# Kernel tuning notes

Measured on AMD Instinct MI355X. Metric: run time of the kernel, lower is better.

## Reference

```python
import jax, jax.numpy as jnp
import numpy as np

N_NODES = 50000
BN_EPS = 1e-5


def setup_inputs() -> dict:
    key = jax.random.key(0)
    ks = jax.random.split(key, 6)
    N, E, CIN, CH, COUT = N_NODES, 800000, 128, 256, 128
    node_feat = jax.random.normal(ks[0], (N, CIN), dtype=jnp.float32)
    edge_index = jax.random.randint(ks[1], (2, E), 0, N, dtype=jnp.int64)
    # Glorot-ish init for weights
    W1 = jax.random.normal(ks[2], (CIN, CH), dtype=jnp.float32) / np.sqrt(CIN)
    b1 = jnp.zeros((CH,), dtype=jnp.float32)
    bn_gamma = jnp.ones((CH,), dtype=jnp.float32)
    bn_beta = jnp.zeros((CH,), dtype=jnp.float32)
    W2 = jax.random.normal(ks[3], (CH, COUT), dtype=jnp.float32) / np.sqrt(CH)
    b2 = jnp.zeros((COUT,), dtype=jnp.float32)
    return {"node_feat": node_feat, "edge_index": edge_index, "W1": W1, "b1": b1,
            "bn_gamma": bn_gamma, "bn_beta": bn_beta, "W2": W2, "b2": b2}


def gcn_conv(x, W, b, src, dst, n_nodes):
    """PyG GCNConv: out = D^-1/2 (A+I) D^-1/2 (x W) + b."""
    h = x @ W                                   # [N, C_out]
    loop = jnp.arange(n_nodes, dtype=src.dtype)
    src_f = jnp.concatenate([src, loop])        # self-loops appended
    dst_f = jnp.concatenate([dst, loop])
    deg = jax.ops.segment_sum(jnp.ones_like(dst_f, dtype=h.dtype), dst_f,
                              num_segments=n_nodes)
    dinv = jax.lax.rsqrt(jnp.maximum(deg, 1.0))  # deg >= 1 due to self-loops
    norm = dinv[src_f] * dinv[dst_f]             # [E+N]
    msg = h[src_f] * norm[:, None]               # gather + scale
    return jax.ops.segment_sum(msg, dst_f, num_segments=n_nodes) + b


def batch_norm(x, gamma, beta):
    mean = jnp.mean(x, axis=0)
    var = jnp.mean((x - mean) ** 2, axis=0)      # biased var (torch BN normalization)
    return (x - mean) * jax.lax.rsqrt(var + BN_EPS) * gamma + beta


def reference(node_feat, edge_index, W1, b1, bn_gamma, bn_beta, W2, b2):
    src, dst = edge_index[0], edge_index[1]
    x = gcn_conv(node_feat, W1, b1, src, dst, N_NODES)
    x = batch_norm(x, bn_gamma, bn_beta)
    x = jax.nn.relu(x)
    # dropout is identity at inference
    x = gcn_conv(x, W2, b2, src, dst, N_NODES)
    return x
```

## Files before the change

### kernel.cpp

```cpp
#include <hip/hip_runtime.h>

#define CIN 128
#define CH 256
#define COUT 128
#define BN_EPS 1e-5f

typedef __attribute__((ext_vector_type(8))) short bf16x8;
typedef __attribute__((ext_vector_type(4))) float f32x4;

__device__ __forceinline__ short f2bf(float x) {
    unsigned u = __float_as_uint(x);
    unsigned r = (u + 0x7fffu + ((u >> 16) & 1u)) >> 16;
    return (short)r;
}
__device__ __forceinline__ float bf2f(short h) {
    return __uint_as_float(((unsigned)(unsigned short)h) << 16);
}

__device__ __forceinline__ void gather_edges(const short* __restrict__ xb,
                                             const uint2* __restrict__ csr,
                                             int e0, int e1, int c,
                                             float* acc) {
    int e = e0;
    for (; e + 7 < e1; e += 8) {
        uint2 ew[8];
        #pragma unroll
        for (int i = 0; i < 8; ++i) ew[i] = csr[e + i];
        bf16x8 x[8];
        #pragma unroll
        for (int i = 0; i < 8; ++i) x[i] = *(const bf16x8*)(xb + (size_t)ew[i].y * 128 + c * 8);
        #pragma unroll
        for (int i = 0; i < 8; ++i) {
            float w = __uint_as_float(ew[i].x);
            #pragma unroll
            for (int j = 0; j < 8; ++j) acc[j] = fmaf(w, bf2f(x[i][j]), acc[j]);
        }
    }
    for (; e + 3 < e1; e += 4) {
        uint2 ew[4];
        #pragma unroll
        for (int i = 0; i < 4; ++i) ew[i] = csr[e + i];
        bf16x8 x[4];
        #pragma unroll
        for (int i = 0; i < 4; ++i) x[i] = *(const bf16x8*)(xb + (size_t)ew[i].y * 128 + c * 8);
        #pragma unroll
        for (int i = 0; i < 4; ++i) {
            float w = __uint_as_float(ew[i].x);
            #pragma unroll
            for (int j = 0; j < 8; ++j) acc[j] = fmaf(w, bf2f(x[i][j]), acc[j]);
        }
    }
    for (; e < e1; ++e) {
        uint2 ew = csr[e];
        float w = __uint_as_float(ew.x);
        bf16x8 x0 = *(const bf16x8*)(xb + (size_t)ew.y * 128 + c * 8);
        #pragma unroll
        for (int j = 0; j < 8; ++j) acc[j] = fmaf(w, bf2f(x0[j]), acc[j]);
    }
}

__global__ void k_deg(const int* __restrict__ dst, int* __restrict__ degi,
                      unsigned short* __restrict__ rank, int E) {
    int e = blockIdx.x * 256 + threadIdx.x;
    if (e < E) rank[e] = (unsigned short)atomicAdd(&degi[dst[e]], 1);
}

__global__ void k_scan1(const int* __restrict__ degi, float* __restrict__ dinv,
                        int* __restrict__ blocksum, int* __restrict__ hist, int N) {
    __shared__ int s[256];
    __shared__ int h[256];
    int tid = threadIdx.x;
    h[tid] = 0;
    int i = blockIdx.x * 256 + tid;
    int v = (i < N) ? degi[i] : 0;
    if (i < N) dinv[i] = rsqrtf((float)(v + 1));
    s[tid] = v;
    __syncthreads();
    if (i < N) atomicAdd(&h[v > 255 ? 255 : v], 1);
    for (int st = 128; st > 0; st >>= 1) {
        if (tid < st) s[tid] += s[tid + st];
        __syncthreads();
    }
    if (tid == 0) blocksum[blockIdx.x] = s[0];
    int hv = h[tid];
    if (hv) atomicAdd(&hist[tid], hv);
}

__global__ void k_scan3(const int* __restrict__ degi, const int* __restrict__ blocksum,
                        int nb, int* __restrict__ rowstart,
                        const int* __restrict__ hist, int* __restrict__ histbase,
                        int N, int E) {
    __shared__ int sb[256];
    __shared__ int s[256];
    int tid = threadIdx.x;
    int bv = (tid < nb) ? blocksum[tid] : 0;
    sb[tid] = bv;
    __syncthreads();
    for (int st = 1; st < 256; st <<= 1) {
        int t = (tid >= st) ? sb[tid - st] : 0;
        __syncthreads();
        sb[tid] += t;
        __syncthreads();
    }
    int boff = (blockIdx.x == 0) ? 0 : sb[blockIdx.x - 1];

    int i = blockIdx.x * 256 + tid;
    int v = (i < N) ? degi[i] : 0;
    s[tid] = v;
    __syncthreads();
    for (int st = 1; st < 256; st <<= 1) {
        int t = (tid >= st) ? s[tid - st] : 0;
        __syncthreads();
        s[tid] += t;
        __syncthreads();
    }
    if (i < N) rowstart[i] = s[tid] - v + boff;
    if (blockIdx.x == 0 && tid == 0) rowstart[N] = E;

    if (blockIdx.x == 0) {
        __shared__ int hh[256];
        int own = hist[tid];
        hh[tid] = own;
        __syncthreads();
        for (int st = 1; st < 256; st <<= 1) {
            int t = (tid >= st) ? hh[tid - st] : 0;
            __syncthreads();
            hh[tid] += t;
            __syncthreads();
        }
        histbase[tid] = hh[tid] - own;
    }
}

__global__ void k_fillperm(const int* __restrict__ src, const int* __restrict__ dst,
                           const unsigned short* __restrict__ rank,
                           const int* __restrict__ rowstart,
                           const float* __restrict__ dinv,
                           uint2* __restrict__ csr,
                           const int* __restrict__ degi,
                           const int* __restrict__ histbase, int* __restrict__ histcnt,
                           int* __restrict__ perm, int E, int N, int nbE) {
    __shared__ int h[256];
    __shared__ int base[256];
    int tid = threadIdx.x;
    if ((int)blockIdx.x < nbE) {
        int e = blockIdx.x * 256 + tid;
        if (e < E) {
            int d = dst[e];
            int s = src[e];
            int pos = rowstart[d] + (int)rank[e];
            uint2 ev;
            ev.x = __float_as_uint(dinv[s] * dinv[d]);
            ev.y = (unsigned)s;
            csr[pos] = ev;
        }
        return;
    }
    int i0 = ((int)blockIdx.x - nbE) * 1024;
    h[tid] = 0;
    __syncthreads();
    int d[4], lr[4];
    #pragma unroll
    for (int k = 0; k < 4; ++k) {
        int i = i0 + k * 256 + tid;
        if (i < N) {
            int dd = degi[i];
            if (dd > 255) dd = 255;
            d[k] = dd;
            lr[k] = atomicAdd(&h[dd], 1);
        } else {
            d[k] = -1;
        }
    }
    __syncthreads();
    int cnt = h[tid];
    if (cnt > 0) base[tid] = atomicAdd(&histcnt[tid], cnt);
    __syncthreads();
    #pragma unroll
    for (int k = 0; k < 4; ++k) {
        if (d[k] >= 0)
            perm[histbase[d[k]] + base[d[k]] + lr[k]] = i0 + k * 256 + tid;
    }
}

__global__ void k_prep(const float* __restrict__ W1, const float* __restrict__ W2,
                       short* __restrict__ W1sw, short* __restrict__ W2sw,
                       const float4* __restrict__ nf, short4* __restrict__ nfb,
                       int* __restrict__ degi, float* __restrict__ stats,
                       int* __restrict__ hist, int n4, int N) {
    int t = blockIdx.x * 256 + threadIdx.x;
    if (t < 32768) {
        if (t < 512) stats[t] = 0.0f;
        else if (t < 1024) hist[t - 512] = 0;
        int n = t >> 7, kk = t & 127;
        float v = W1[kk * 256 + n];
        int t16 = n >> 4, m = n & 15;
        int ks = kk >> 5, q = (kk >> 3) & 3, j = kk & 7;
        W1sw[(t16 * 4 + ks) * 512 + (q * 16 + m) * 8 + j] = f2bf(v);
    } else if (t < 65536) {
        int u = t - 32768;
        int n = u >> 8, kk = u & 255;
        float v = W2[kk * 128 + n];
        int t16 = n >> 4, m = n & 15;
        int ks = kk >> 5, q = (kk >> 3) & 3, j = kk & 7;
        W2sw[(t16 * 8 + ks) * 512 + (q * 16 + m) * 8 + j] = f2bf(v);
    } else {
        int u = t - 65536;
        if (u < n4) {
            float4 v = nf[u];
            short4 s;
            s.x = f2bf(v.x); s.y = f2bf(v.y); s.z = f2bf(v.z); s.w = f2bf(v.w);
            nfb[u] = s;
        } else {
            int u2 = u - n4;
            if (u2 < N) degi[u2] = 0;
        }
    }
}

__global__ __launch_bounds__(512, 4) void k_gemm1g(
        const short* __restrict__ xb, const int* __restrict__ rowstart,
        const uint2* __restrict__ csr, const float* __restrict__ dinv,
        const int* __restrict__ perm, const short* __restrict__ Bsw,
        const float* __restrict__ bias, short* __restrict__ C,
        float* __restrict__ stats, int M) {
    constexpr int K = CIN, NOUT = CH;
    constexpr int CT = NOUT / 128;
    constexpr int KS = K / 32;
    constexpr int KP = K + 8;
    constexpr int LROW = NOUT + 8;
    constexpr int LSZ = (64 * KP > 64 * LROW) ? 64 * KP : 64 * LROW;
    __shared__ __align__(16) short lds[LSZ];
    __shared__ int prow[64];
    int tid = threadIdx.x;
    int wave = tid >> 6;
    int lane = tid & 63;
    int m = lane & 15;
    int q = lane >> 4;
    int row0 = blockIdx.x * 64;
    if (tid < 64) {
        int pos = row0 + tid;
        if (pos >= M) pos = M - 1;
        prow[tid] = perm[M - 1 - pos];
    }
    __syncthreads();

    int c = tid & 15;
    int g = tid >> 4;
    #pragma unroll
    for (int p = 0; p < 2; ++p) {
        int rl = p * 32 + g;
        int r = prow[rl];
        float di = dinv[r];
        float w0 = di * di;
        bf16x8 sv = *(const bf16x8*)(xb + (size_t)r * 128 + c * 8);
        float acc[8];
        #pragma unroll
        for (int j = 0; j < 8; ++j) acc[j] = bf2f(sv[j]) * w0;
        gather_edges(xb, csr, rowstart[r], rowstart[r + 1], c, acc);
        bf16x8 h;
        #pragma unroll
        for (int j = 0; j < 8; ++j) h[j] = f2bf(acc[j]);
        *(bf16x8*)(lds + rl * KP + c * 8) = h;
    }
    __syncthreads();

    f32x4 acc4[4][CT];
    #pragma unroll
    for (int rt = 0; rt < 4; ++rt)
        #pragma unroll
        for (int ct = 0; ct < CT; ++ct)
            acc4[rt][ct] = (f32x4){0.f, 0.f, 0.f, 0.f};

    #pragma unroll
    for (int ks = 0; ks < KS; ++ks) {
        bf16x8 bh[CT];
        #pragma unroll
        for (int ct = 0; ct < CT; ++ct)
            bh[ct] = *(const bf16x8*)(Bsw + (size_t)((wave * CT + ct) * KS + ks) * 512 + lane * 8);
        bf16x8 af[4];
        #pragma unroll
        for (int rt = 0; rt < 4; ++rt)
            af[rt] = *(const bf16x8*)(lds + (rt * 16 + m) * KP + ks * 32 + q * 8);
        #pragma unroll
        for (int ct = 0; ct < CT; ++ct)
            #pragma unroll
            for (int rt = 0; rt < 4; ++rt)
                acc4[rt][ct] = __builtin_amdgcn_mfma_f32_16x16x32_bf16(af[rt], bh[ct], acc4[rt][ct], 0, 0, 0);
    }
    __syncthreads();

    #pragma unroll
    for (int ct = 0; ct < CT; ++ct) {
        int col = wave * 32 + ct * 16 + m;
        float bv = bias[col];
        float s = 0.f, sq = 0.f;
        #pragma unroll
        for (int rt = 0; rt < 4; ++rt) {
            #pragma unroll
            for (int r = 0; r < 4; ++r) {
                int lrow = rt * 16 + q * 4 + r;
                float v = acc4[rt][ct][r] + bv;
                if (row0 + lrow < M) { s += v; sq = fmaf(v, v, sq); }
                lds[lrow * LROW + col] = f2bf(v);
            }
        }
        s += __shfl_xor(s, 16, 64);
        s += __shfl_xor(s, 32, 64);
        sq += __shfl_xor(sq, 16, 64);
        sq += __shfl_xor(sq, 32, 64);
        if (lane < 16) {
            unsafeAtomicAdd(&stats[col], s);
            unsafeAtomicAdd(&stats[256 + col], sq);
        }
    }
    __syncthreads();
    constexpr int CPR = NOUT / 8;
    #pragma unroll
    for (int i = 0; i < (64 * CPR) / 512; ++i) {
        int idx = i * 512 + tid;
        int row = idx / CPR;
        int ch = idx % CPR;
        if (row0 + row < M)
            *(bf16x8*)(C + (size_t)prow[row] * NOUT + ch * 8) =
                *(const bf16x8*)(lds + row * LROW + ch * 8);
    }
}

__device__ __forceinline__ bf16x8 bnrelu8(bf16x8 raw, const float* __restrict__ scsh, int c) {
    float4 sc0 = *(const float4*)(scsh + c);
    float4 sc1 = *(const float4*)(scsh + c + 4);
    float4 sh0 = *(const float4*)(scsh + 256 + c);
    float4 sh1 = *(const float4*)(scsh + 256 + c + 4);
    bf16x8 o;
    o[0] = f2bf(fmaxf(fmaf(bf2f(raw[0]), sc0.x, sh0.x), 0.f));
    o[1] = f2bf(fmaxf(fmaf(bf2f(raw[1]), sc0.y, sh0.y), 0.f));
    o[2] = f2bf(fmaxf(fmaf(bf2f(raw[2]), sc0.z, sh0.z), 0.f));
    o[3] = f2bf(fmaxf(fmaf(bf2f(raw[3]), sc0.w, sh0.w), 0.f));
    o[4] = f2bf(fmaxf(fmaf(bf2f(raw[4]), sc1.x, sh1.x), 0.f));
    o[5] = f2bf(fmaxf(fmaf(bf2f(raw[5]), sc1.y, sh1.y), 0.f));
    o[6] = f2bf(fmaxf(fmaf(bf2f(raw[6]), sc1.z, sh1.z), 0.f));
    o[7] = f2bf(fmaxf(fmaf(bf2f(raw[7]), sc1.w, sh1.w), 0.f));
    return o;
}

__global__ __launch_bounds__(256, 4) void k_gemm2(
        const short* __restrict__ A, const short* __restrict__ Bsw,
        const float* __restrict__ stats, const float* __restrict__ gamma,
        const float* __restrict__ beta, short* __restrict__ C, int M) {
    constexpr int K = CH, NOUT = COUT;
    constexpr int CT = NOUT / 64;
    constexpr int KS = K / 32;
    constexpr int KP = K + 8;
    constexpr int LROW = NOUT + 8;
    constexpr int LSZ = (64 * KP > 64 * LROW) ? 64 * KP : 64 * LROW;
    __shared__ __align__(16) short lds[LSZ];
    __shared__ float scsh[512];
    int tid = threadIdx.x;
    int wave = tid >> 6;
    int lane = tid & 63;
    int m = lane & 15;
    int q = lane >> 4;
    int row0 = blockIdx.x * 64;

    if (tid < 256) {
        float invN = 1.0f / (float)M;
        float mean = stats[tid] * invN;
        float var = fmaxf(stats[256 + tid] * invN - mean * mean, 0.f);
        float inv = rsqrtf(var + BN_EPS);
        float sc = gamma[tid] * inv;
        scsh[tid] = sc;
        scsh[256 + tid] = fmaf(-mean, sc, beta[tid]);
    }
    __syncthreads();

    constexpr int CPRA = K / 8;
    #pragma unroll
    for (int i = 0; i < (64 * CPRA) / 256; ++i) {
        int idx = i * 256 + tid;
        int r = idx / CPRA, cc = idx % CPRA;
        int gr = row0 + r;
        if (gr >= M) gr = M - 1;
        bf16x8 v = *(const bf16x8*)(A + (size_t)gr * K + cc * 8);
        v = bnrelu8(v, scsh, cc * 8);
        *(bf16x8*)(lds + r * KP + cc * 8) = v;
    }
    __syncthreads();

    f32x4 acc[4][CT];
    #pragma unroll
    for (int rt = 0; rt < 4; ++rt)
        #pragma unroll
        for (int ct = 0; ct < CT; ++ct)
            acc[rt][ct] = (f32x4){0.f, 0.f, 0.f, 0.f};

    #pragma unroll
    for (int ks = 0; ks < KS; ++ks) {
        bf16x8 bh[CT];
        #pragma unroll
        for (int ct = 0; ct < CT; ++ct)
            bh[ct] = *(const bf16x8*)(Bsw + (size_t)((wave * CT + ct) * KS + ks) * 512 + lane * 8);
        bf16x8 af[4];
        #pragma unroll
        for (int rt = 0; rt < 4; ++rt)
            af[rt] = *(const bf16x8*)(lds + (rt * 16 + m) * KP + ks * 32 + q * 8);
        #pragma unroll
        for (int ct = 0; ct < CT; ++ct)
            #pragma unroll
            for (int rt = 0; rt < 4; ++rt)
                acc[rt][ct] = __builtin_amdgcn_mfma_f32_16x16x32_bf16(af[rt], bh[ct], acc[rt][ct], 0, 0, 0);
    }
    __syncthreads();

    #pragma unroll
    for (int ct = 0; ct < CT; ++ct) {
        int col = wave * (NOUT / 4) + ct * 16 + m;
        #pragma unroll
        for (int rt = 0; rt < 4; ++rt) {
            #pragma unroll
            for (int r = 0; r < 4; ++r) {
                int lrow = rt * 16 + q * 4 + r;
                lds[lrow * LROW + col] = f2bf(acc[rt][ct][r]);
            }
        }
    }
    __syncthreads();
    constexpr int CPR = NOUT / 8;
    #pragma unroll
    for (int i = 0; i < (64 * CPR) / 256; ++i) {
        int idx = i * 256 + tid;
        int row = idx / CPR;
        int ch = idx % CPR;
        if (row0 + row < M)
            *(bf16x8*)(C + (size_t)(row0 + row) * NOUT + ch * 8) =
                *(const bf16x8*)(lds + row * LROW + ch * 8);
    }
}

__global__ __launch_bounds__(256) void k_gather1(
        const short* __restrict__ yb, const int* __restrict__ rowstart,
        const uint2* __restrict__ csr, const float* __restrict__ dinv,
        const int* __restrict__ perm, const float* __restrict__ bias,
        float* __restrict__ out, int N) {
    int t = blockIdx.x * 256 + threadIdx.x;
    int sp = t >> 4;
    int c = t & 15;
    if (sp >= N) return;
    int r = perm[N - 1 - sp];
    float di = dinv[r];
    float w0 = di * di;
    bf16x8 sv = *(const bf16x8*)(yb + (size_t)r * 128 + c * 8);
    float acc[8];
    #pragma unroll
    for (int j = 0; j < 8; ++j) acc[j] = bf2f(sv[j]) * w0;
    gather_edges(yb, csr, rowstart[r], rowstart[r + 1], c, acc);
    float4 b0 = *(const float4*)(bias + c * 8);
    float4 b1 = *(const float4*)(bias + c * 8 + 4);
    float4 o0 = make_float4(acc[0] + b0.x, acc[1] + b0.y, acc[2] + b0.z, acc[3] + b0.w);
    float4 o1 = make_float4(acc[4] + b1.x, acc[5] + b1.y, acc[6] + b1.z, acc[7] + b1.w);
    *(float4*)(out + (size_t)r * 128 + c * 8) = o0;
    *(float4*)(out + (size_t)r * 128 + c * 8 + 4) = o1;
}

extern "C" void kernel_launch(void* const* d_in, const int* in_sizes, int n_in,
                              void* d_out, int out_size, void* d_ws, size_t ws_size,
                              hipStream_t stream) {
    const float* nf    = (const float*)d_in[0];
    const int*   ei    = (const int*)d_in[1];
    const float* W1    = (const float*)d_in[2];
    const float* b1    = (const float*)d_in[3];
    const float* gamma = (const float*)d_in[4];
    const float* beta  = (const float*)d_in[5];
    const float* W2    = (const float*)d_in[6];
    const float* b2    = (const float*)d_in[7];
    float* out = (float*)d_out;

    const int N = in_sizes[0] / CIN;
    const int E = in_sizes[1] / 2;
    const int* src = ei;
    const int* dst = ei + E;

    const int nb1 = (N + 63) / 64;

    char* ws = (char*)d_ws;
    auto align256 = [](size_t x) { return (x + 255) & ~(size_t)255; };
    size_t off = 0;
    int*   degi = (int*)(ws + off);      off += align256((size_t)N * 4);
    float* stats = (float*)(ws + off);   off += align256(512 * 4);
    float* dinv = (float*)(ws + off);    off += align256((size_t)N * 4);
    int*   rowstart = (int*)(ws + off);  off += align256((size_t)(N + 1) * 4);
    int*   blocksum = (int*)(ws + off);  off += align256(256 * 4);
    int*   hist = (int*)(ws + off);      off += align256(512 * 4);
    int*   histbase = (int*)(ws + off);  off += align256(256 * 4);
    int*   perm = (int*)(ws + off);      off += align256((size_t)N * 4);
    short* W1sw = (short*)(ws + off);    off += align256(32768 * 2);
    short* W2sw = (short*)(ws + off);    off += align256(32768 * 2);
    unsigned short* rank = (unsigned short*)(ws + off); off += align256((size_t)E * 2);
    uint2* csr = (uint2*)(ws + off);     off += align256((size_t)E * 8);
    short* nfb = (short*)(ws + off);     off += align256((size_t)N * CIN * 2);
    short* x1b = (short*)(ws + off);     off += align256((size_t)N * CH * 2);
    short* yb = (short*)(ws + off);      off += align256((size_t)N * COUT * 2);

    int nbN = (N + 255) / 256;
    int nbE = (E + 255) / 256;
    int nbP = (N + 1023) / 1024;
    int n4 = N * 32;

    k_prep<<<(65536 + n4 + N + 255) / 256, 256, 0, stream>>>(
        W1, W2, W1sw, W2sw, (const float4*)nf, (short4*)nfb, degi, stats, hist, n4, N);

    k_deg<<<nbE, 256, 0, stream>>>(dst, degi, rank, E);
    k_scan1<<<nbN, 256, 0, stream>>>(degi, dinv, blocksum, hist, N);
    k_scan3<<<nbN, 256, 0, stream>>>(degi, blocksum, nbN, rowstart, hist, histbase, N, E);
    k_fillperm<<<nbE + nbP, 256, 0, stream>>>(
        src, dst, rank, rowstart, dinv, csr, degi, histbase, hist + 256, perm, E, N, nbE);

    k_gemm1g<<<nb1, 512, 0, stream>>>(nfb, rowstart, csr, dinv, perm, W1sw, b1, x1b, stats, N);

    k_gemm2<<<nb1, 256, 0, stream>>>(x1b, W2sw, stats, gamma, beta, yb, N);

    k_gather1<<<(N * 16 + 255) / 256, 256, 0, stream>>>(
        yb, rowstart, csr, dinv, perm, b2, out, N);
}
```

Baseline: 242.4 us.

## Fuse both GEMM stages into one cooperative persistent kernel with grid sync

Merges the first-layer gather+GEMM and the BN+ReLU+second GEMM into a single cooperative kernel. A grid-wide barrier separates BN statistics accumulation from their use. Each block keeps its last tile in LDS and spills the others to a workspace buffer, which avoids one global round trip and one launch. Tiles now pair high-degree and low-degree rows to balance gather work across blocks. The cost is a grid sync, a persistent grid capped by occupancy, and some duplicated overlap rows that are written twice.

```diff
diff --git a/kernel.cpp b/kernel.cpp
--- a/kernel.cpp
+++ b/kernel.cpp
@@ -1,4 +1,7 @@
 #include <hip/hip_runtime.h>
+#include <hip/hip_cooperative_groups.h>
+
+namespace cg = cooperative_groups;
 
 #define CIN 128
 #define CH 256
@@ -218,115 +221,6 @@
     }
 }
 
-__global__ __launch_bounds__(512, 4) void k_gemm1g(
-        const short* __restrict__ xb, const int* __restrict__ rowstart,
-        const uint2* __restrict__ csr, const float* __restrict__ dinv,
-        const int* __restrict__ perm, const short* __restrict__ Bsw,
-        const float* __restrict__ bias, short* __restrict__ C,
-        float* __restrict__ stats, int M) {
-    constexpr int K = CIN, NOUT = CH;
-    constexpr int CT = NOUT / 128;
-    constexpr int KS = K / 32;
-    constexpr int KP = K + 8;
-    constexpr int LROW = NOUT + 8;
-    constexpr int LSZ = (64 * KP > 64 * LROW) ? 64 * KP : 64 * LROW;
-    __shared__ __align__(16) short lds[LSZ];
-    __shared__ int prow[64];
-    int tid = threadIdx.x;
-    int wave = tid >> 6;
-    int lane = tid & 63;
-    int m = lane & 15;
-    int q = lane >> 4;
-    int row0 = blockIdx.x * 64;
-    if (tid < 64) {
-        int pos = row0 + tid;
-        if (pos >= M) pos = M - 1;
-        prow[tid] = perm[M - 1 - pos];
-    }
-    __syncthreads();
-
-    int c = tid & 15;
-    int g = tid >> 4;
-    #pragma unroll
-    for (int p = 0; p < 2; ++p) {
-        int rl = p * 32 + g;
-        int r = prow[rl];
-        float di = dinv[r];
-        float w0 = di * di;
-        bf16x8 sv = *(const bf16x8*)(xb + (size_t)r * 128 + c * 8);
-        float acc[8];
-        #pragma unroll
-        for (int j = 0; j < 8; ++j) acc[j] = bf2f(sv[j]) * w0;
-        gather_edges(xb, csr, rowstart[r], rowstart[r + 1], c, acc);
-        bf16x8 h;
-        #pragma unroll
-        for (int j = 0; j < 8; ++j) h[j] = f2bf(acc[j]);
-        *(bf16x8*)(lds + rl * KP + c * 8) = h;
-    }
-    __syncthreads();
-
-    f32x4 acc4[4][CT];
-    #pragma unroll
-    for (int rt = 0; rt < 4; ++rt)
-        #pragma unroll
-        for (int ct = 0; ct < CT; ++ct)
-            acc4[rt][ct] = (f32x4){0.f, 0.f, 0.f, 0.f};
-
-    #pragma unroll
-    for (int ks = 0; ks < KS; ++ks) {
-        bf16x8 bh[CT];
-        #pragma unroll
-        for (int ct = 0; ct < CT; ++ct)
-            bh[ct] = *(const bf16x8*)(Bsw + (size_t)((wave * CT + ct) * KS + ks) * 512 + lane * 8);
-        bf16x8 af[4];
-        #pragma unroll
-        for (int rt = 0; rt < 4; ++rt)
-            af[rt] = *(const bf16x8*)(lds + (rt * 16 + m) * KP + ks * 32 + q * 8);
-        #pragma unroll
-        for (int ct = 0; ct < CT; ++ct)
-            #pragma unroll
-            for (int rt = 0; rt < 4; ++rt)
-                acc4[rt][ct] = __builtin_amdgcn_mfma_f32_16x16x32_bf16(af[rt], bh[ct], acc4[rt][ct], 0, 0, 0);
-    }
-    __syncthreads();
-
-    #pragma unroll
-    for (int ct = 0; ct < CT; ++ct) {
-        int col = wave * 32 + ct * 16 + m;
-        float bv = bias[col];
-        float s = 0.f, sq = 0.f;
-        #pragma unroll
-        for (int rt = 0; rt < 4; ++rt) {
-            #pragma unroll
-            for (int r = 0; r < 4; ++r) {
-                int lrow = rt * 16 + q * 4 + r;
-                float v = acc4[rt][ct][r] + bv;
-                if (row0 + lrow < M) { s += v; sq = fmaf(v, v, sq); }
-                lds[lrow * LROW + col] = f2bf(v);
-            }
-        }
-        s += __shfl_xor(s, 16, 64);
-        s += __shfl_xor(s, 32, 64);
-        sq += __shfl_xor(sq, 16, 64);
-        sq += __shfl_xor(sq, 32, 64);
-        if (lane < 16) {
-            unsafeAtomicAdd(&stats[col], s);
-            unsafeAtomicAdd(&stats[256 + col], sq);
-        }
-    }
-    __syncthreads();
-    constexpr int CPR = NOUT / 8;
-    #pragma unroll
-    for (int i = 0; i < (64 * CPR) / 512; ++i) {
-        int idx = i * 512 + tid;
-        int row = idx / CPR;
-        int ch = idx % CPR;
-        if (row0 + row < M)
-            *(bf16x8*)(C + (size_t)prow[row] * NOUT + ch * 8) =
-                *(const bf16x8*)(lds + row * LROW + ch * 8);
-    }
-}
-
 __device__ __forceinline__ bf16x8 bnrelu8(bf16x8 raw, const float* __restrict__ scsh, int c) {
     float4 sc0 = *(const float4*)(scsh + c);
     float4 sc1 = *(const float4*)(scsh + c + 4);
@@ -344,24 +238,122 @@
     return o;
 }
 
-__global__ __launch_bounds__(256, 4) void k_gemm2(
-        const short* __restrict__ A, const short* __restrict__ Bsw,
-        const float* __restrict__ stats, const float* __restrict__ gamma,
-        const float* __restrict__ beta, short* __restrict__ C, int M) {
-    constexpr int K = CH, NOUT = COUT;
-    constexpr int CT = NOUT / 64;
-    constexpr int KS = K / 32;
-    constexpr int KP = K + 8;
-    constexpr int LROW = NOUT + 8;
-    constexpr int LSZ = (64 * KP > 64 * LROW) ? 64 * KP : 64 * LROW;
-    __shared__ __align__(16) short lds[LSZ];
+__global__ __launch_bounds__(512, 4) void k_fused(
+        const short* __restrict__ xb, const int* __restrict__ rowstart,
+        const uint2* __restrict__ csr, const float* __restrict__ dinv,
+        const int* __restrict__ perm, const short* __restrict__ W1sw,
+        const short* __restrict__ W2sw, const float* __restrict__ b1,
+        const float* __restrict__ gamma, const float* __restrict__ beta,
+        short* __restrict__ yb, short* __restrict__ spill,
+        float* __restrict__ stats, int M, int NT) {
+    constexpr int KP = CIN + 8;
+    constexpr int LROW = CH + 8;
+    __shared__ __align__(16) short lds[64 * LROW];
     __shared__ float scsh[512];
+    __shared__ int prow[64];
+    cg::grid_group grid = cg::this_grid();
     int tid = threadIdx.x;
     int wave = tid >> 6;
     int lane = tid & 63;
     int m = lane & 15;
     int q = lane >> 4;
-    int row0 = blockIdx.x * 64;
+    int b = blockIdx.x;
+    int G = gridDim.x;
+    int lightN = M - 32 * NT;
+    int lastT = b + ((NT - 1 - b) / G) * G;
+
+    for (int t = b; t < NT; t += G) {
+        if (tid < 64) {
+            prow[tid] = (tid < 32) ? perm[M - 1 - (t * 32 + tid)]
+                                   : perm[t * 32 + (tid - 32)];
+        }
+        __syncthreads();
+
+        int c = tid & 15;
+        int g = tid >> 4;
+        #pragma unroll
+        for (int p = 0; p < 2; ++p) {
+            int rl = p * 32 + g;
+            int r = prow[rl];
+            float di = dinv[r];
+            float w0 = di * di;
+            bf16x8 sv = *(const bf16x8*)(xb + (size_t)r * 128 + c * 8);
+            float acc[8];
+            #pragma unroll
+            for (int j = 0; j < 8; ++j) acc[j] = bf2f(sv[j]) * w0;
+            gather_edges(xb, csr, rowstart[r], rowstart[r + 1], c, acc);
+            bf16x8 h;
+            #pragma unroll
+            for (int j = 0; j < 8; ++j) h[j] = f2bf(acc[j]);
+            *(bf16x8*)(lds + rl * KP + c * 8) = h;
+        }
+        __syncthreads();
+
+        f32x4 acc4[4][2];
+        #pragma unroll
+        for (int rt = 0; rt < 4; ++rt)
+            #pragma unroll
+            for (int ct = 0; ct < 2; ++ct)
+                acc4[rt][ct] = (f32x4){0.f, 0.f, 0.f, 0.f};
+
+        #pragma unroll
+        for (int ks = 0; ks < 4; ++ks) {
+            bf16x8 bh[2];
+            #pragma unroll
+            for (int ct = 0; ct < 2; ++ct)
+                bh[ct] = *(const bf16x8*)(W1sw + (size_t)((wave * 2 + ct) * 4 + ks) * 512 + lane * 8);
+            bf16x8 af[4];
+            #pragma unroll
+            for (int rt = 0; rt < 4; ++rt)
+                af[rt] = *(const bf16x8*)(lds + (rt * 16 + m) * KP + ks * 32 + q * 8);
+            #pragma unroll
+            for (int ct = 0; ct < 2; ++ct)
+                #pragma unroll
+                for (int rt = 0; rt < 4; ++rt)
+                    acc4[rt][ct] = __builtin_amdgcn_mfma_f32_16x16x32_bf16(af[rt], bh[ct], acc4[rt][ct], 0, 0, 0);
+        }
+        __syncthreads();
+
+        #pragma unroll
+        for (int ct = 0; ct < 2; ++ct) {
+            int col = wave * 32 + ct * 16 + m;
+            float bv = b1[col];
+            float s = 0.f, sq = 0.f;
+            #pragma unroll
+            for (int rt = 0; rt < 4; ++rt) {
+                #pragma unroll
+                for (int r = 0; r < 4; ++r) {
+                    int lrow = rt * 16 + q * 4 + r;
+                    float v = acc4[rt][ct][r] + bv;
+                    bool cnt = (lrow < 32) || (t * 32 + lrow - 32 < lightN);
+                    if (cnt) { s += v; sq = fmaf(v, v, sq); }
+                    lds[lrow * LROW + col] = f2bf(v);
+                }
+            }
+            s += __shfl_xor(s, 16, 64);
+            s += __shfl_xor(s, 32, 64);
+            sq += __shfl_xor(sq, 16, 64);
+            sq += __shfl_xor(sq, 32, 64);
+            if (lane < 16) {
+                unsafeAtomicAdd(&stats[col], s);
+                unsafeAtomicAdd(&stats[256 + col], sq);
+            }
+        }
+        __syncthreads();
+
+        if (t != lastT) {
+            #pragma unroll
+            for (int i = 0; i < 4; ++i) {
+                int idx = i * 512 + tid;
+                int r = idx >> 5, cc = idx & 31;
+                *(bf16x8*)(spill + (size_t)t * (64 * 256) + r * 256 + cc * 8) =
+                    *(const bf16x8*)(lds + r * LROW + cc * 8);
+            }
+        }
+    }
+
+    __threadfence();
+    grid.sync();
 
     if (tid < 256) {
         float invN = 1.0f / (float)M;
@@ -372,72 +364,72 @@
         scsh[tid] = sc;
         scsh[256 + tid] = fmaf(-mean, sc, beta[tid]);
     }
-    __syncthreads();
-
-    constexpr int CPRA = K / 8;
-    #pragma unroll
-    for (int i = 0; i < (64 * CPRA) / 256; ++i) {
-        int idx = i * 256 + tid;
-        int r = idx / CPRA, cc = idx % CPRA;
-        int gr = row0 + r;
-        if (gr >= M) gr = M - 1;
-        bf16x8 v = *(const bf16x8*)(A + (size_t)gr * K + cc * 8);
-        v = bnrelu8(v, scsh, cc * 8);
-        *(bf16x8*)(lds + r * KP + cc * 8) = v;
-    }
-    __syncthreads();
-
-    f32x4 acc[4][CT];
-    #pragma unroll
-    for (int rt = 0; rt < 4; ++rt)
-        #pragma unroll
-        for (int ct = 0; ct < CT; ++ct)
-            acc[rt][ct] = (f32x4){0.f, 0.f, 0.f, 0.f};
-
-    #pragma unroll
-    for (int ks = 0; ks < KS; ++ks) {
-        bf16x8 bh[CT];
-        #pragma unroll
-        for (int ct = 0; ct < CT; ++ct)
-            bh[ct] = *(const bf16x8*)(Bsw + (size_t)((wave * CT + ct) * KS + ks) * 512 + lane * 8);
-        bf16x8 af[4];
-        #pragma unroll
-        for (int rt = 0; rt < 4; ++rt)
-            af[rt] = *(const bf16x8*)(lds + (rt * 16 + m) * KP + ks * 32 + q * 8);
-        #pragma unroll
-        for (int ct = 0; ct < CT; ++ct)
+
+    bool inLDS = true;
+    for (int t = lastT; t >= b; t -= G) {
+        __syncthreads();
+        if (tid < 64) {
+            prow[tid] = (tid < 32) ? perm[M - 1 - (t * 32 + tid)]
+                                   : perm[t * 32 + (tid - 32)];
+        }
+        if (!inLDS) {
+            #pragma unroll
+            for (int i = 0; i < 4; ++i) {
+                int idx = i * 512 + tid;
+                int r = idx >> 5, cc = idx & 31;
+                *(bf16x8*)(lds + r * LROW + cc * 8) =
+                    *(const bf16x8*)(spill + (size_t)t * (64 * 256) + r * 256 + cc * 8);
+            }
+        }
+        __syncthreads();
+
+        #pragma unroll
+        for (int i = 0; i < 4; ++i) {
+            int idx = i * 512 + tid;
+            int r = idx >> 5, cc = idx & 31;
+            bf16x8 v = *(const bf16x8*)(lds + r * LROW + cc * 8);
+            v = bnrelu8(v, scsh, cc * 8);
+            *(bf16x8*)(lds + r * LROW + cc * 8) = v;
+        }
+        __syncthreads();
+
+        f32x4 a2[4];
+        #pragma unroll
+        for (int rt = 0; rt < 4; ++rt) a2[rt] = (f32x4){0.f, 0.f, 0.f, 0.f};
+        #pragma unroll
+        for (int ks = 0; ks < 8; ++ks) {
+            bf16x8 bh = *(const bf16x8*)(W2sw + (size_t)((wave * 8 + ks) * 512) + lane * 8);
+            bf16x8 af[4];
             #pragma unroll
             for (int rt = 0; rt < 4; ++rt)
-                acc[rt][ct] = __builtin_amdgcn_mfma_f32_16x16x32_bf16(af[rt], bh[ct], acc[rt][ct], 0, 0, 0);
-    }
-    __syncthreads();
-
-    #pragma unroll
-    for (int ct = 0; ct < CT; ++ct) {
-        int col = wave * (NOUT / 4) + ct * 16 + m;
-        #pragma unroll
-        for (int rt = 0; rt < 4; ++rt) {
-            #pragma unroll
-            for (int r = 0; r < 4; ++r) {
-                int lrow = rt * 16 + q * 4 + r;
-                lds[lrow * LROW + col] = f2bf(acc[rt][ct][r]);
-            }
-        }
-    }
-    __syncthreads();
-    constexpr int CPR = NOUT / 8;
-    #pragma unroll
-    for (int i = 0; i < (64 * CPR) / 256; ++i) {
-        int idx = i * 256 + tid;
-        int row = idx / CPR;
-        int ch = idx % CPR;
-        if (row0 + row < M)
-            *(bf16x8*)(C + (size_t)(row0 + row) * NOUT + ch * 8) =
-                *(const bf16x8*)(lds + row * LROW + ch * 8);
-    }
-}
-
-__global__ __launch_bounds__(256) void k_gather1(
+                af[rt] = *(const bf16x8*)(lds + (rt * 16 + m) * LROW + ks * 32 + q * 8);
+            #pragma unroll
+            for (int rt = 0; rt < 4; ++rt)
+                a2[rt] = __builtin_amdgcn_mfma_f32_16x16x32_bf16(af[rt], bh, a2[rt], 0, 0, 0);
+        }
+        __syncthreads();
+
+        {
+            int col = wave * 16 + m;
+            #pragma unroll
+            for (int rt = 0; rt < 4; ++rt)
+                #pragma unroll
+                for (int r = 0; r < 4; ++r)
+                    lds[(rt * 16 + q * 4 + r) * 136 + col] = f2bf(a2[rt][r]);
+        }
+        __syncthreads();
+        #pragma unroll
+        for (int i = 0; i < 2; ++i) {
+            int idx = i * 512 + tid;
+            int row = idx >> 4, ch = idx & 15;
+            *(bf16x8*)(yb + (size_t)prow[row] * 128 + ch * 8) =
+                *(const bf16x8*)(lds + row * 136 + ch * 8);
+        }
+        inLDS = false;
+    }
+}
+
+__global__ __launch_bounds__(256, 4) void k_gather1(
         const short* __restrict__ yb, const int* __restrict__ rowstart,
         const uint2* __restrict__ csr, const float* __restrict__ dinv,
         const int* __restrict__ perm, const float* __restrict__ bias,
@@ -480,7 +472,7 @@
     const int* src = ei;
     const int* dst = ei + E;
 
-    const int nb1 = (N + 63) / 64;
+    const int NT = (N + 63) / 64;
 
     char* ws = (char*)d_ws;
     auto align256 = [](size_t x) { return (x + 255) & ~(size_t)255; };
@@ -498,7 +490,7 @@
     unsigned short* rank = (unsigned short*)(ws + off); off += align256((size_t)E * 2);
     uint2* csr = (uint2*)(ws + off);     off += align256((size_t)E * 8);
     short* nfb = (short*)(ws + off);     off += align256((size_t)N * CIN * 2);
-    short* x1b = (short*)(ws + off);     off += align256((size_t)N * CH * 2);
+    short* spill = (short*)(ws + off);   off += align256((size_t)NT * 64 * 256 * 2);
     short* yb = (short*)(ws + off);      off += align256((size_t)N * COUT * 2);
 
     int nbN = (N + 255) / 256;
@@ -515,9 +507,22 @@
     k_fillperm<<<nbE + nbP, 256, 0, stream>>>(
         src, dst, rank, rowstart, dinv, csr, degi, histbase, hist + 256, perm, E, N, nbE);
 
-    k_gemm1g<<<nb1, 512, 0, stream>>>(nfb, rowstart, csr, dinv, perm, W1sw, b1, x1b, stats, N);
-
-    k_gemm2<<<nb1, 256, 0, stream>>>(x1b, W2sw, stats, gamma, beta, yb, N);
+    static int maxB = -1;
+    if (maxB < 0) {
+        hipError_t oe = hipOccupancyMaxActiveBlocksPerMultiprocessor(&maxB, k_fused, 512, 0);
+        if (oe != hipSuccess || maxB < 1) maxB = 1;
+    }
+    int cap = maxB * 256;
+    int G = (NT < cap) ? NT : cap;
+    {
+        int M2 = N, NT2 = NT;
+        void* kargs[] = {(void*)&nfb, (void*)&rowstart, (void*)&csr, (void*)&dinv,
+                         (void*)&perm, (void*)&W1sw, (void*)&W2sw, (void*)&b1,
+                         (void*)&gamma, (void*)&beta, (void*)&yb, (void*)&spill,
+                         (void*)&stats, (void*)&M2, (void*)&NT2};
+        hipLaunchCooperativeKernel(reinterpret_cast<void*>(k_fused),
+                                   dim3(G), dim3(512), kargs, 0, stream);
+    }
 
     k_gather1<<<(N * 16 + 255) / 256, 256, 0, stream>>>(
         yb, rowstart, csr, dinv, perm, b2, out, N);
```

New measurement: 349.4 us. 44.1% more time.
